# Optimization experiments

Hardware: AMD Instinct MI355X
Metric: run time of the kernel (lower is better)

## Reference

```python
import jax, jax.numpy as jnp
import numpy as np

B, S, D = 4, 2048, 1024
ATTN_D, OUT_D, H = 1024, 1024, 16
EPS = 1e-12


def setup_inputs() -> dict:
    key = jax.random.key(0)
    ks = jax.random.split(key, 9)
    s = 0.02
    return {
        "x": jax.random.normal(ks[0], (B, S, D), dtype=jnp.float32),
        "wq": jax.random.normal(ks[1], (D, ATTN_D), dtype=jnp.float32) * s,
        "bq": jnp.zeros((ATTN_D,), dtype=jnp.float32),
        "wk": jax.random.normal(ks[2], (D, ATTN_D), dtype=jnp.float32) * s,
        "bk": jnp.zeros((ATTN_D,), dtype=jnp.float32),
        "wv": jax.random.normal(ks[3], (D, ATTN_D), dtype=jnp.float32) * s,
        "bv": jnp.zeros((ATTN_D,), dtype=jnp.float32),
        "wo": jax.random.normal(ks[4], (ATTN_D, OUT_D), dtype=jnp.float32) * s,
        "bo": jnp.zeros((OUT_D,), dtype=jnp.float32),
        "ln_g": jnp.ones((OUT_D,), dtype=jnp.float32),
        "ln_b": jnp.zeros((OUT_D,), dtype=jnp.float32),
    }


def reference(x, wq, bq, wk, bk, wv, bv, wo, bo, ln_g, ln_b):
    b, s, _ = x.shape
    hd = ATTN_D // H  # head_dim
    # projections -> [B, H, S, hd]
    q = (x @ wq + bq).reshape(b, s, H, hd).transpose(0, 2, 1, 3)
    k = (x @ wk + bk).reshape(b, s, H, hd).transpose(0, 2, 1, 3)
    v = (x @ wv + bv).reshape(b, s, H, hd).transpose(0, 2, 1, 3)
    # full O(S^2) score matrix, as in the original module
    scores = jnp.einsum("bhqd,bhkd->bhqk", q, k) / jnp.sqrt(jnp.float32(hd))
    attn = jax.nn.softmax(scores, axis=-1)
    out = jnp.einsum("bhqk,bhkd->bhqd", attn, v)
    out = out.transpose(0, 2, 1, 3).reshape(b, s, ATTN_D)
    out = out @ wo + bo
    # LayerNorm (no residual in this module)
    mu = jnp.mean(out, axis=-1, keepdims=True)
    var = jnp.var(out, axis=-1, keepdims=True)
    out = (out - mu) * jax.lax.rsqrt(var + EPS) * ln_g + ln_b
    return out
```

## Files before the change

### kernel.cpp

```cpp
#include <hip/hip_runtime.h>

typedef __bf16 bf16;
typedef __bf16 bf16x4 __attribute__((ext_vector_type(4)));
typedef __bf16 bf16x8 __attribute__((ext_vector_type(8)));
typedef float f32x4 __attribute__((ext_vector_type(4)));

#define NB 4
#define NS 2048
#define ND 1024
#define NH 16
#define HD 64

#define QSCALE 0.18033688f

__device__ __forceinline__ void gload_lds16(const void* g, void* l) {
  __builtin_amdgcn_global_load_lds(
      (const __attribute__((address_space(1))) void*)g,
      (__attribute__((address_space(3))) void*)l, 16, 0, 0);
}

__device__ __forceinline__ float fast_exp2(float x) {
#if __has_builtin(__builtin_amdgcn_exp2f)
  return __builtin_amdgcn_exp2f(x);
#else
  return exp2f(x);
#endif
}

__global__ __launch_bounds__(256) void k_cvt(const float* __restrict__ src,
                                             bf16* __restrict__ dst) {
  size_t i = ((size_t)blockIdx.x * 256 + threadIdx.x) * 4;
  float4 v = *(const float4*)(src + i);
  bf16x4 o = {(__bf16)v.x, (__bf16)v.y, (__bf16)v.z, (__bf16)v.w};
  *(bf16x4*)(dst + i) = o;
}

__global__ __launch_bounds__(256) void k_cvt_T(const float* __restrict__ src,
                                               bf16* __restrict__ dst) {
  __shared__ float t[32][33];
  int tx = threadIdx.x, ty = threadIdx.y;
  int x = blockIdx.x * 32 + tx;
  int y = blockIdx.y * 32 + ty;
#pragma unroll
  for (int j = 0; j < 4; ++j)
    t[ty + j * 8][tx] = src[(size_t)(y + j * 8) * 1024 + x];
  __syncthreads();
  int x2 = blockIdx.y * 32 + tx;
  int y2 = blockIdx.x * 32 + ty;
#pragma unroll
  for (int j = 0; j < 4; ++j)
    dst[(size_t)(y2 + j * 8) * 1024 + x2] = (__bf16)t[tx][ty + j * 8];
}

__global__ __launch_bounds__(256) void k_vT(const bf16* __restrict__ V,
                                            bf16* __restrict__ Vt) {
  __shared__ bf16 t[64][72];
  int tid = threadIdx.x;
  int bh = blockIdx.x >> 5, st = blockIdx.x & 31;
  const bf16* src = V + ((size_t)bh * NS + st * 64) * HD;
#pragma unroll
  for (int rep = 0; rep < 2; ++rep) {
    int idx = rep * 256 + tid;
    int r = idx >> 3, c8 = (idx & 7) * 8;
    *(bf16x8*)&t[r][c8] = *(const bf16x8*)(src + (size_t)r * HD + c8);
  }
  __syncthreads();
  bf16* dst = Vt + (size_t)bh * HD * NS + st * 64;
#pragma unroll
  for (int rep = 0; rep < 2; ++rep) {
    int idx = rep * 256 + tid;
    int d = idx >> 3, s8 = (idx & 7) * 8;
    bf16x8 v;
#pragma unroll
    for (int j = 0; j < 8; ++j) {
      int jj = (j + tid) & 7;
      v[jj] = t[s8 + jj][d];
    }
    *(bf16x8*)(dst + (size_t)d * NS + s8) = v;
  }
}

__device__ __forceinline__ void gemm_mainloop(const bf16* __restrict__ A,
                                              const bf16* __restrict__ BT,
                                              int bm, int bn, int K,
                                              bf16* sA, bf16* sB,
                                              f32x4 acc[4][4]) {
  const int tid = threadIdx.x;
  const int w = tid >> 6, lane = tid & 63, quad = lane >> 4, l15 = lane & 15;
  const int wm = (w >> 1) * 64, wn = (w & 1) * 64;
  const bf16* ga = A + (size_t)(bm * 128 + (tid >> 2)) * K + (tid & 3) * 8;
  const bf16* gb = BT + (size_t)(bn * 128 + (tid >> 2)) * K + (tid & 3) * 8;
  bf16* lA0 = sA + w * 512;
  bf16* lA1 = sA + 2048 + w * 512;
  bf16* lB0 = sB + w * 512;
  bf16* lB1 = sB + 2048 + w * 512;
  const int kiter = K >> 5;
  for (int kt = 0; kt < kiter; ++kt) {
    gload_lds16(ga, lA0);
    gload_lds16(ga + (size_t)64 * K, lA1);
    gload_lds16(gb, lB0);
    gload_lds16(gb + (size_t)64 * K, lB1);
    ga += 32;
    gb += 32;
    __syncthreads();
    bf16x8 av[4], bv[4];
#pragma unroll
    for (int i = 0; i < 4; ++i)
      av[i] = *(const bf16x8*)(sA + (wm + i * 16 + l15) * 32 + quad * 8);
#pragma unroll
    for (int i = 0; i < 4; ++i)
      bv[i] = *(const bf16x8*)(sB + (wn + i * 16 + l15) * 32 + quad * 8);
#pragma unroll
    for (int mi = 0; mi < 4; ++mi)
#pragma unroll
      for (int ni = 0; ni < 4; ++ni)
        acc[mi][ni] = __builtin_amdgcn_mfma_f32_16x16x32_bf16(
            av[mi], bv[ni], acc[mi][ni], 0, 0, 0);
    __syncthreads();
  }
}

__global__ __launch_bounds__(256) void k_gemm_qkv(
    const bf16* __restrict__ A, const bf16* __restrict__ BT,
    const float* __restrict__ bq, const float* __restrict__ bk,
    const float* __restrict__ bv, bf16* __restrict__ Q, bf16* __restrict__ K,
    bf16* __restrict__ V) {
  __shared__ alignas(16) bf16 sA[4096];
  __shared__ alignas(16) bf16 sB[4096];
  f32x4 acc[4][4] = {};
  const int bm = blockIdx.y, bn = blockIdx.x;
  gemm_mainloop(A, BT, bm, bn, 1024, sA, sB, acc);
  const int tid = threadIdx.x;
  const int w = tid >> 6, lane = tid & 63, quad = lane >> 4, l15 = lane & 15;
  const int wm = (w >> 1) * 64, wn = (w & 1) * 64;
#pragma unroll
  for (int ni = 0; ni < 4; ++ni) {
    int col = bn * 128 + wn + ni * 16 + l15;
    int which = col >> 10, nn = col & 1023;
    int h = nn >> 6, d = nn & 63;
    const float* bias = which == 0 ? bq : which == 1 ? bk : bv;
    bf16* dst = which == 0 ? Q : which == 1 ? K : V;
    float bb = bias[nn];
    float scl = which == 0 ? QSCALE : 1.f;
#pragma unroll
    for (int mi = 0; mi < 4; ++mi) {
      int row = bm * 128 + wm + mi * 16 + quad * 4;
#pragma unroll
      for (int r = 0; r < 4; ++r) {
        int rr = row + r;
        int b = rr >> 11, s = rr & 2047;
        dst[(((size_t)b * NH + h) * NS + s) * HD + d] =
            (__bf16)((acc[mi][ni][r] + bb) * scl);
      }
    }
  }
}

__global__ __launch_bounds__(256) void k_gemm_out(const bf16* __restrict__ A,
                                                  const bf16* __restrict__ BT,
                                                  const float* __restrict__ bo,
                                                  float* __restrict__ Y) {
  __shared__ alignas(16) bf16 sA[4096];
  __shared__ alignas(16) bf16 sB[4096];
  f32x4 acc[4][4] = {};
  const int bm = blockIdx.y, bn = blockIdx.x;
  gemm_mainloop(A, BT, bm, bn, 1024, sA, sB, acc);
  const int tid = threadIdx.x;
  const int w = tid >> 6, lane = tid & 63, quad = lane >> 4, l15 = lane & 15;
  const int wm = (w >> 1) * 64, wn = (w & 1) * 64;
#pragma unroll
  for (int ni = 0; ni < 4; ++ni) {
    int col = bn * 128 + wn + ni * 16 + l15;
    float bb = bo[col];
#pragma unroll
    for (int mi = 0; mi < 4; ++mi) {
      int row = bm * 128 + wm + mi * 16 + quad * 4;
#pragma unroll
      for (int r = 0; r < 4; ++r)
        Y[(size_t)(row + r) * 1024 + col] = acc[mi][ni][r] + bb;
    }
  }
}

__global__ __launch_bounds__(256, 2) void k_attn(const bf16* __restrict__ Qg,
                                                 const bf16* __restrict__ Kg,
                                                 const bf16* __restrict__ VtG,
                                                 bf16* __restrict__ O) {
  __shared__ alignas(16) char smem[49152];
  bf16* sK = (bf16*)smem;
  bf16* sVt = (bf16*)(smem + 8192);
  const int tid = threadIdx.x;
  const int w = tid >> 6, lane = tid & 63, quad = lane >> 4, l15 = lane & 15;
  const int l7 = l15 & 7, l8 = lane >> 3;
  const int bh = blockIdx.x >> 3;
  const int qt = blockIdx.x & 7;
  const bf16* Qh = Qg + (size_t)bh * NS * HD;
  const bf16* Kh = Kg + (size_t)bh * NS * HD;
  const bf16* Vh = VtG + (size_t)bh * HD * NS;
  bf16* Pw = (bf16*)(smem + 16384) + w * 4096;

  const int q0 = qt * 256 + w * 64;
  bf16x8 qb[4][2];
#pragma unroll
  for (int ni = 0; ni < 4; ++ni)
#pragma unroll
    for (int ks = 0; ks < 2; ++ks)
      qb[ni][ks] = *(const bf16x8*)(Qh + (size_t)(q0 + ni * 16 + l15) * HD +
                                    ks * 32 + quad * 8);

  const int gsw = ((lane & 7) ^ l8) * 8;
  const bf16* gk = Kh + (size_t)(w * 8 + l8) * HD + gsw;
  const bf16* gv = Vh + (size_t)(w * 8 + l8) * NS + gsw;
  bf16* dk0 = sK + w * 512;
  bf16* dk1 = sK + (4 + w) * 512;
  bf16* dv0 = sVt + w * 512;
  bf16* dv1 = sVt + (4 + w) * 512;

  f32x4 o_acc[4][4] = {};
  float l_run[4] = {0.f, 0.f, 0.f, 0.f};

  int offA[4][2], offP[2][4];
#pragma unroll
  for (int mi = 0; mi < 4; ++mi)
#pragma unroll
    for (int ks = 0; ks < 2; ++ks)
      offA[mi][ks] = (mi * 16 + l15) * 64 + (((ks * 4 + quad) ^ l7) * 8);
#pragma unroll
  for (int ks = 0; ks < 2; ++ks)
#pragma unroll
    for (int ni = 0; ni < 4; ++ni)
      offP[ks][ni] = (ni * 16 + l15) * 64 + (((ks * 4 + quad) ^ l7) * 8);

  for (int c = 0; c < NS; c += 64) {
    __syncthreads();
    gload_lds16(gk, dk0);
    gload_lds16(gk + 32 * HD, dk1);
    gload_lds16(gv, dv0);
    gload_lds16(gv + 32 * NS, dv1);
    gk += 64 * HD;
    gv += 64;
    __syncthreads();

#pragma unroll
    for (int mi = 0; mi < 4; ++mi) {
      f32x4 s[4] = {};
#pragma unroll
      for (int ks = 0; ks < 2; ++ks) {
        bf16x8 ak = *(const bf16x8*)(sK + offA[mi][ks]);
#pragma unroll
        for (int ni = 0; ni < 4; ++ni)
          s[ni] = __builtin_amdgcn_mfma_f32_16x16x32_bf16(ak, qb[ni][ks],
                                                          s[ni], 0, 0, 0);
      }
#pragma unroll
      for (int ni = 0; ni < 4; ++ni) {
#pragma unroll
        for (int r = 0; r < 4; ++r) {
          s[ni][r] = fast_exp2(s[ni][r]);
          l_run[ni] += s[ni][r];
        }
        bf16x4 p = {(__bf16)s[ni][0], (__bf16)s[ni][1], (__bf16)s[ni][2],
                    (__bf16)s[ni][3]};
        *(bf16x4*)(Pw + (ni * 16 + l15) * 64 +
                   (((2 * mi + (quad >> 1)) ^ l7) * 8) + (quad & 1) * 4) = p;
      }
    }

#pragma unroll
    for (int ks = 0; ks < 2; ++ks) {
      bf16x8 pb[4];
#pragma unroll
      for (int ni = 0; ni < 4; ++ni)
        pb[ni] = *(const bf16x8*)(Pw + offP[ks][ni]);
#pragma unroll
      for (int mi = 0; mi < 4; ++mi) {
        bf16x8 av = *(const bf16x8*)(sVt + offA[mi][ks]);
#pragma unroll
        for (int ni = 0; ni < 4; ++ni)
          o_acc[mi][ni] = __builtin_amdgcn_mfma_f32_16x16x32_bf16(
              av, pb[ni], o_acc[mi][ni], 0, 0, 0);
      }
    }
  }

  int b = bh >> 4, h = bh & 15;
#pragma unroll
  for (int ni = 0; ni < 4; ++ni) {
    float l = l_run[ni];
    l += __shfl_xor(l, 16, 64);
    l += __shfl_xor(l, 32, 64);
    float inv = 1.f / l;
    int q = q0 + ni * 16 + l15;
    size_t orow = ((size_t)b * NS + q) * 1024 + h * 64;
#pragma unroll
    for (int mi = 0; mi < 4; ++mi) {
      bf16x4 ov = {
          (__bf16)(o_acc[mi][ni][0] * inv), (__bf16)(o_acc[mi][ni][1] * inv),
          (__bf16)(o_acc[mi][ni][2] * inv), (__bf16)(o_acc[mi][ni][3] * inv)};
      *(bf16x4*)(O + orow + mi * 16 + quad * 4) = ov;
    }
  }
}

__global__ __launch_bounds__(256) void k_ln(float* __restrict__ Y,
                                            const float* __restrict__ g,
                                            const float* __restrict__ bta) {
  int row = blockIdx.x, tid = threadIdx.x;
  float4 v = ((const float4*)(Y + (size_t)row * 1024))[tid];
  float sm = v.x + v.y + v.z + v.w;
  float sq = v.x * v.x + v.y * v.y + v.z * v.z + v.w * v.w;
#pragma unroll
  for (int off = 1; off < 64; off <<= 1) {
    sm += __shfl_xor(sm, off, 64);
    sq += __shfl_xor(sq, off, 64);
  }
  __shared__ float red[8];
  int w = tid >> 6, lane = tid & 63;
  if (lane == 0) {
    red[w] = sm;
    red[4 + w] = sq;
  }
  __syncthreads();
  sm = red[0] + red[1] + red[2] + red[3];
  sq = red[4] + red[5] + red[6] + red[7];
  float mu = sm * (1.f / 1024.f);
  float var = sq * (1.f / 1024.f) - mu * mu;
  float rstd = rsqrtf(var + 1e-12f);
  float4 g4 = ((const float4*)g)[tid];
  float4 b4 = ((const float4*)bta)[tid];
  float4 o;
  o.x = (v.x - mu) * rstd * g4.x + b4.x;
  o.y = (v.y - mu) * rstd * g4.y + b4.y;
  o.z = (v.z - mu) * rstd * g4.z + b4.z;
  o.w = (v.w - mu) * rstd * g4.w + b4.w;
  ((float4*)(Y + (size_t)row * 1024))[tid] = o;
}

extern "C" void kernel_launch(void* const* d_in, const int* in_sizes, int n_in,
                              void* d_out, int out_size, void* d_ws,
                              size_t ws_size, hipStream_t stream) {
  const float* x = (const float*)d_in[0];
  const float* wq = (const float*)d_in[1];
  const float* bq = (const float*)d_in[2];
  const float* wk = (const float*)d_in[3];
  const float* bk = (const float*)d_in[4];
  const float* wv = (const float*)d_in[5];
  const float* bv = (const float*)d_in[6];
  const float* wo = (const float*)d_in[7];
  const float* bo = (const float*)d_in[8];
  const float* ln_g = (const float*)d_in[9];
  const float* ln_b = (const float*)d_in[10];
  float* out = (float*)d_out;

  char* ws = (char*)d_ws;
  bf16* xb = (bf16*)ws;          ws += 16777216;
  bf16* wqkvT = (bf16*)ws;       ws += 6291456;
  bf16* woT = (bf16*)ws;         ws += 2097152;
  bf16* Qh = (bf16*)ws;          ws += 16777216;
  bf16* Kh = (bf16*)ws;          ws += 16777216;
  bf16* Vh = (bf16*)ws;          ws += 16777216;
  bf16* Vt = (bf16*)ws;          ws += 16777216;
  bf16* AOb = (bf16*)ws;         ws += 16777216;

  k_cvt<<<8192, 256, 0, stream>>>(x, xb);
  dim3 tb(32, 8);
  k_cvt_T<<<dim3(32, 32), tb, 0, stream>>>(wq, wqkvT);
  k_cvt_T<<<dim3(32, 32), tb, 0, stream>>>(wk, wqkvT + 1024 * 1024);
  k_cvt_T<<<dim3(32, 32), tb, 0, stream>>>(wv, wqkvT + 2 * 1024 * 1024);
  k_cvt_T<<<dim3(32, 32), tb, 0, stream>>>(wo, woT);

  k_gemm_qkv<<<dim3(24, 64), 256, 0, stream>>>(xb, wqkvT, bq, bk, bv, Qh, Kh,
                                               Vh);
  k_vT<<<NB * NH * 32, 256, 0, stream>>>(Vh, Vt);
  k_attn<<<NB * NH * (NS / 256), 256, 0, stream>>>(Qh, Kh, Vt, AOb);
  k_gemm_out<<<dim3(8, 64), 256, 0, stream>>>(AOb, woT, bo, out);
  k_ln<<<8192, 256, 0, stream>>>(out, ln_g, ln_b);
}
```

Before: 308.4 us.

## Stage GEMM epilogues through LDS, double-buffer attention K/V, merge weight conversions

The QKV GEMM epilogue now stages each warp's tile in shared memory and writes Q/K/V as coalesced 16-byte rows in [B,S,H*D] layout, replacing scattered per-element head-major stores. The attention and V-transpose kernels are updated to read that strided layout. The output GEMM stages through LDS to issue float4 stores. The attention loop double-buffers K/V tiles, prefetching the next chunk while computing the current one, and the block order is changed so consecutive blocks cover different heads. The four weight-transpose launches are merged into one. The costs are more shared memory per block (64KB in attention, which may reduce occupancy) and strided Q/K reads in attention.

After: 295.5 us. 4.2% less time.

```diff
diff --git a/kernel.cpp b/kernel.cpp
--- a/kernel.cpp
+++ b/kernel.cpp
@@ -35,8 +35,15 @@
   *(bf16x4*)(dst + i) = o;
 }
 
-__global__ __launch_bounds__(256) void k_cvt_T(const float* __restrict__ src,
-                                               bf16* __restrict__ dst) {
+__global__ __launch_bounds__(256) void k_cvt_T4(const float* __restrict__ wq,
+                                                const float* __restrict__ wk,
+                                                const float* __restrict__ wv,
+                                                const float* __restrict__ wo,
+                                                bf16* __restrict__ wqkvT,
+                                                bf16* __restrict__ woT) {
+  int z = blockIdx.z;
+  const float* src = z == 0 ? wq : z == 1 ? wk : z == 2 ? wv : wo;
+  bf16* dst = z < 3 ? wqkvT + (size_t)z * 1048576 : woT;
   __shared__ float t[32][33];
   int tx = threadIdx.x, ty = threadIdx.y;
   int x = blockIdx.x * 32 + tx;
@@ -57,12 +64,13 @@
   __shared__ bf16 t[64][72];
   int tid = threadIdx.x;
   int bh = blockIdx.x >> 5, st = blockIdx.x & 31;
-  const bf16* src = V + ((size_t)bh * NS + st * 64) * HD;
+  int b = bh >> 4, h = bh & 15;
+  const bf16* src = V + ((size_t)b * NS + st * 64) * ND + h * HD;
 #pragma unroll
   for (int rep = 0; rep < 2; ++rep) {
     int idx = rep * 256 + tid;
     int r = idx >> 3, c8 = (idx & 7) * 8;
-    *(bf16x8*)&t[r][c8] = *(const bf16x8*)(src + (size_t)r * HD + c8);
+    *(bf16x8*)&t[r][c8] = *(const bf16x8*)(src + (size_t)r * ND + c8);
   }
   __syncthreads();
   bf16* dst = Vt + (size_t)bh * HD * NS + st * 64;
@@ -127,32 +135,36 @@
     bf16* __restrict__ V) {
   __shared__ alignas(16) bf16 sA[4096];
   __shared__ alignas(16) bf16 sB[4096];
+  __shared__ alignas(16) bf16 sE[4 * 64 * 72];
   f32x4 acc[4][4] = {};
   const int bm = blockIdx.y, bn = blockIdx.x;
   gemm_mainloop(A, BT, bm, bn, 1024, sA, sB, acc);
   const int tid = threadIdx.x;
   const int w = tid >> 6, lane = tid & 63, quad = lane >> 4, l15 = lane & 15;
   const int wm = (w >> 1) * 64, wn = (w & 1) * 64;
+  bf16* sEw = sE + w * 64 * 72;
+  const int colbase = bn * 128 + wn;
+  const int which = colbase >> 10;
+  const int nnbase = colbase & 1023;
+  const float* bias = which == 0 ? bq : which == 1 ? bk : bv;
+  bf16* dst = which == 0 ? Q : which == 1 ? K : V;
+  const float scl = which == 0 ? QSCALE : 1.f;
 #pragma unroll
   for (int ni = 0; ni < 4; ++ni) {
-    int col = bn * 128 + wn + ni * 16 + l15;
-    int which = col >> 10, nn = col & 1023;
-    int h = nn >> 6, d = nn & 63;
-    const float* bias = which == 0 ? bq : which == 1 ? bk : bv;
-    bf16* dst = which == 0 ? Q : which == 1 ? K : V;
-    float bb = bias[nn];
-    float scl = which == 0 ? QSCALE : 1.f;
-#pragma unroll
-    for (int mi = 0; mi < 4; ++mi) {
-      int row = bm * 128 + wm + mi * 16 + quad * 4;
-#pragma unroll
-      for (int r = 0; r < 4; ++r) {
-        int rr = row + r;
-        int b = rr >> 11, s = rr & 2047;
-        dst[(((size_t)b * NH + h) * NS + s) * HD + d] =
+    float bb = bias[nnbase + ni * 16 + l15];
+#pragma unroll
+    for (int mi = 0; mi < 4; ++mi)
+#pragma unroll
+      for (int r = 0; r < 4; ++r)
+        sEw[(mi * 16 + quad * 4 + r) * 72 + ni * 16 + l15] =
             (__bf16)((acc[mi][ni][r] + bb) * scl);
-      }
-    }
+  }
+  const int l8 = lane >> 3, g8 = (lane & 7) * 8;
+#pragma unroll
+  for (int i = 0; i < 8; ++i) {
+    int row = i * 8 + l8;
+    bf16x8 vv = *(const bf16x8*)(sEw + row * 72 + g8);
+    *(bf16x8*)(dst + (size_t)(bm * 128 + wm + row) * 1024 + nnbase + g8) = vv;
   }
 }
 
@@ -162,22 +174,35 @@
                                                   float* __restrict__ Y) {
   __shared__ alignas(16) bf16 sA[4096];
   __shared__ alignas(16) bf16 sB[4096];
+  __shared__ alignas(16) float sE[4 * 32 * 68];
   f32x4 acc[4][4] = {};
   const int bm = blockIdx.y, bn = blockIdx.x;
   gemm_mainloop(A, BT, bm, bn, 1024, sA, sB, acc);
   const int tid = threadIdx.x;
   const int w = tid >> 6, lane = tid & 63, quad = lane >> 4, l15 = lane & 15;
   const int wm = (w >> 1) * 64, wn = (w & 1) * 64;
-#pragma unroll
-  for (int ni = 0; ni < 4; ++ni) {
-    int col = bn * 128 + wn + ni * 16 + l15;
-    float bb = bo[col];
-#pragma unroll
-    for (int mi = 0; mi < 4; ++mi) {
-      int row = bm * 128 + wm + mi * 16 + quad * 4;
-#pragma unroll
-      for (int r = 0; r < 4; ++r)
-        Y[(size_t)(row + r) * 1024 + col] = acc[mi][ni][r] + bb;
+  float* sEw = sE + w * 32 * 68;
+  const int colbase = bn * 128 + wn;
+  float bb[4];
+#pragma unroll
+  for (int ni = 0; ni < 4; ++ni) bb[ni] = bo[colbase + ni * 16 + l15];
+  const int l4 = lane >> 4, c4 = (lane & 15) * 4;
+#pragma unroll
+  for (int h2 = 0; h2 < 2; ++h2) {
+#pragma unroll
+    for (int ml = 0; ml < 2; ++ml)
+#pragma unroll
+      for (int ni = 0; ni < 4; ++ni)
+#pragma unroll
+        for (int r = 0; r < 4; ++r)
+          sEw[(ml * 16 + quad * 4 + r) * 68 + ni * 16 + l15] =
+              acc[h2 * 2 + ml][ni][r] + bb[ni];
+#pragma unroll
+    for (int i = 0; i < 8; ++i) {
+      int row = i * 4 + l4;
+      float4 v = *(const float4*)(sEw + row * 68 + c4);
+      *(float4*)(Y + (size_t)(bm * 128 + wm + h2 * 32 + row) * 1024 + colbase +
+                 c4) = v;
     }
   }
 }
@@ -186,18 +211,19 @@
                                                  const bf16* __restrict__ Kg,
                                                  const bf16* __restrict__ VtG,
                                                  bf16* __restrict__ O) {
-  __shared__ alignas(16) char smem[49152];
+  __shared__ alignas(16) char smem[65536];
   bf16* sK = (bf16*)smem;
-  bf16* sVt = (bf16*)(smem + 8192);
+  bf16* sVt = (bf16*)(smem + 16384);
   const int tid = threadIdx.x;
   const int w = tid >> 6, lane = tid & 63, quad = lane >> 4, l15 = lane & 15;
   const int l7 = l15 & 7, l8 = lane >> 3;
-  const int bh = blockIdx.x >> 3;
-  const int qt = blockIdx.x & 7;
-  const bf16* Qh = Qg + (size_t)bh * NS * HD;
-  const bf16* Kh = Kg + (size_t)bh * NS * HD;
+  const int bh = blockIdx.x & 63;
+  const int qt = blockIdx.x >> 6;
+  const int b = bh >> 4, h = bh & 15;
+  const bf16* Qh = Qg + (size_t)b * NS * ND + h * HD;
+  const bf16* Kh = Kg + (size_t)b * NS * ND + h * HD;
   const bf16* Vh = VtG + (size_t)bh * HD * NS;
-  bf16* Pw = (bf16*)(smem + 16384) + w * 4096;
+  bf16* Pw = (bf16*)(smem + 32768) + w * 4096;
 
   const int q0 = qt * 256 + w * 64;
   bf16x8 qb[4][2];
@@ -205,16 +231,14 @@
   for (int ni = 0; ni < 4; ++ni)
 #pragma unroll
     for (int ks = 0; ks < 2; ++ks)
-      qb[ni][ks] = *(const bf16x8*)(Qh + (size_t)(q0 + ni * 16 + l15) * HD +
+      qb[ni][ks] = *(const bf16x8*)(Qh + (size_t)(q0 + ni * 16 + l15) * ND +
                                     ks * 32 + quad * 8);
 
   const int gsw = ((lane & 7) ^ l8) * 8;
-  const bf16* gk = Kh + (size_t)(w * 8 + l8) * HD + gsw;
+  const bf16* gk = Kh + (size_t)(w * 8 + l8) * ND + gsw;
   const bf16* gv = Vh + (size_t)(w * 8 + l8) * NS + gsw;
-  bf16* dk0 = sK + w * 512;
-  bf16* dk1 = sK + (4 + w) * 512;
-  bf16* dv0 = sVt + w * 512;
-  bf16* dv1 = sVt + (4 + w) * 512;
+  bf16* dk = sK + w * 512;
+  bf16* dv = sVt + w * 512;
 
   f32x4 o_acc[4][4] = {};
   float l_run[4] = {0.f, 0.f, 0.f, 0.f};
@@ -231,22 +255,30 @@
     for (int ni = 0; ni < 4; ++ni)
       offP[ks][ni] = (ni * 16 + l15) * 64 + (((ks * 4 + quad) ^ l7) * 8);
 
-  for (int c = 0; c < NS; c += 64) {
+  gload_lds16(gk, dk);
+  gload_lds16(gk + 32 * ND, dk + 2048);
+  gload_lds16(gv, dv);
+  gload_lds16(gv + 32 * NS, dv + 2048);
+
+  for (int it = 0; it < NS / 64; ++it) {
+    const int buf = (it & 1) * 4096;
     __syncthreads();
-    gload_lds16(gk, dk0);
-    gload_lds16(gk + 32 * HD, dk1);
-    gload_lds16(gv, dv0);
-    gload_lds16(gv + 32 * NS, dv1);
-    gk += 64 * HD;
-    gv += 64;
-    __syncthreads();
+    if (it + 1 < NS / 64) {
+      const int nbuf = 4096 - buf;
+      const bf16* gk1 = gk + (size_t)(it + 1) * 64 * ND;
+      const bf16* gv1 = gv + (it + 1) * 64;
+      gload_lds16(gk1, dk + nbuf);
+      gload_lds16(gk1 + 32 * ND, dk + nbuf + 2048);
+      gload_lds16(gv1, dv + nbuf);
+      gload_lds16(gv1 + 32 * NS, dv + nbuf + 2048);
+    }
 
 #pragma unroll
     for (int mi = 0; mi < 4; ++mi) {
       f32x4 s[4] = {};
 #pragma unroll
       for (int ks = 0; ks < 2; ++ks) {
-        bf16x8 ak = *(const bf16x8*)(sK + offA[mi][ks]);
+        bf16x8 ak = *(const bf16x8*)(sK + buf + offA[mi][ks]);
 #pragma unroll
         for (int ni = 0; ni < 4; ++ni)
           s[ni] = __builtin_amdgcn_mfma_f32_16x16x32_bf16(ak, qb[ni][ks],
@@ -274,7 +306,7 @@
         pb[ni] = *(const bf16x8*)(Pw + offP[ks][ni]);
 #pragma unroll
       for (int mi = 0; mi < 4; ++mi) {
-        bf16x8 av = *(const bf16x8*)(sVt + offA[mi][ks]);
+        bf16x8 av = *(const bf16x8*)(sVt + buf + offA[mi][ks]);
 #pragma unroll
         for (int ni = 0; ni < 4; ++ni)
           o_acc[mi][ni] = __builtin_amdgcn_mfma_f32_16x16x32_bf16(
@@ -283,7 +315,6 @@
     }
   }
 
-  int b = bh >> 4, h = bh & 15;
 #pragma unroll
   for (int ni = 0; ni < 4; ++ni) {
     float l = l_run[ni];
@@ -364,10 +395,7 @@
 
   k_cvt<<<8192, 256, 0, stream>>>(x, xb);
   dim3 tb(32, 8);
-  k_cvt_T<<<dim3(32, 32), tb, 0, stream>>>(wq, wqkvT);
-  k_cvt_T<<<dim3(32, 32), tb, 0, stream>>>(wk, wqkvT + 1024 * 1024);
-  k_cvt_T<<<dim3(32, 32), tb, 0, stream>>>(wv, wqkvT + 2 * 1024 * 1024);
-  k_cvt_T<<<dim3(32, 32), tb, 0, stream>>>(wo, woT);
+  k_cvt_T4<<<dim3(32, 32, 4), tb, 0, stream>>>(wq, wk, wv, wo, wqkvT, woT);
 
   k_gemm_qkv<<<dim3(24, 64), 256, 0, stream>>>(xb, wqkvT, bq, bk, bv, Qh, Kh,
                                                Vh);
```
